# Kernel tuning notes

Measured on AMD Instinct MI355X. Metric: run time of the kernel, lower is better.

## Reference

```python
import jax, jax.numpy as jnp
import numpy as np

D_MODEL = 4096
N_EXPERTS = 64
LN_EPS = 1e-5


def setup_inputs() -> dict:
    key = jax.random.key(0)
    k_x, k_w, k_b = jax.random.split(key, 3)
    x = jax.random.normal(k_x, (4, 4096, D_MODEL), dtype=jnp.float32)
    # LayerNorm affine params (torch defaults: ones / zeros)
    gamma = jnp.ones((D_MODEL,), dtype=jnp.float32)
    beta = jnp.zeros((D_MODEL,), dtype=jnp.float32)
    # Linear(d_model, n): weight (n, d), bias (n) — kaiming-uniform-ish init
    bound = 1.0 / np.sqrt(D_MODEL)
    W = jax.random.uniform(k_w, (N_EXPERTS, D_MODEL), dtype=jnp.float32, minval=-bound, maxval=bound)
    b = jax.random.uniform(k_b, (N_EXPERTS,), dtype=jnp.float32, minval=-bound, maxval=bound)
    return {"x": x, "gamma": gamma, "beta": beta, "W": W, "b": b, "top_k": 2}


def reference(x, gamma, beta, W, b, top_k):
    # LayerNorm over last dim
    mu = jnp.mean(x, axis=-1, keepdims=True)
    var = jnp.mean(jnp.square(x - mu), axis=-1, keepdims=True)
    xn = (x - mu) * jax.lax.rsqrt(var + LN_EPS) * gamma + beta
    # Gate projection: (B,T,d) @ (d,n) -> (B,T,n)
    logits = jnp.einsum('btd,nd->btn', xn, W) + b
    weights = jax.nn.softmax(logits, axis=-1)  # (B,T,n)
    k = min(int(top_k), weights.shape[-1])
    topk_vals, indices = jax.lax.top_k(weights, k)  # (B,T,k)
    # scatter top-k values back to dense (B,T,n), then renormalize
    onehot = jax.nn.one_hot(indices, weights.shape[-1], dtype=weights.dtype)  # (B,T,k,n)
    sparse_w = jnp.einsum('btkn,btk->btn', onehot, topk_vals)
    sparse_w = sparse_w / (jnp.sum(sparse_w, axis=-1, keepdims=True) + 1e-8)
    # load-balance (entropy) loss on dense weights
    mean_w = jnp.mean(weights, axis=(0, 1))  # (n,)
    lb_loss = -jnp.sum(mean_w * jnp.log(mean_w + 1e-8))
    return sparse_w, indices, lb_loss
```

## Files before the change

### kernel.cpp

```cpp
#include <hip/hip_runtime.h>
#include <math.h>

#define D_MODEL 4096
#define N_EXP   64
#define N_ROWS  16384
#define LN_EPS  1e-5f
#define TMB     64
#define NBLK    (N_ROWS / TMB)

typedef __attribute__((ext_vector_type(4))) float f32x4;
typedef __attribute__((ext_vector_type(8))) short s16x8;

struct U4 { unsigned v[4]; };

__device__ __forceinline__ unsigned pkt(float a, float b) {
  unsigned ua = __builtin_bit_cast(unsigned, a);
  unsigned ub = __builtin_bit_cast(unsigned, b);
  return (ua >> 16) | (ub & 0xffff0000u);
}
__device__ __forceinline__ float lo2f(unsigned p) { return __builtin_bit_cast(float, p << 16); }
__device__ __forceinline__ float hi2f(unsigned p) { return __builtin_bit_cast(float, p & 0xffff0000u); }

__device__ __forceinline__ void split8(const float* f, U4& u1, U4& u2, U4& u3) {
#pragma unroll
  for (int i = 0; i < 4; ++i) {
    const float a = f[2 * i], b = f[2 * i + 1];
    const unsigned p1 = pkt(a, b);
    const float ra = a - lo2f(p1), rb = b - hi2f(p1);
    const unsigned p2 = pkt(ra, rb);
    const float sa = ra - lo2f(p2), sb = rb - hi2f(p2);
    u1.v[i] = p1; u2.v[i] = p2; u3.v[i] = pkt(sa, sb);
  }
}


__global__ __launch_bounds__(64) void prep_bpre(
    const float* __restrict__ W, const float* __restrict__ gamma,
    float* __restrict__ Bpre)
{
  const int b = blockIdx.x;
  const int kb32 = b >> 2, j0 = b & 3;
  const int L = threadIdx.x, q = L >> 4, c = L & 15;
  const int n  = j0 * 16 + c;
  const int k0 = kb32 * 32 + q * 8;
  const float4 w0 = *(const float4*)(W + (size_t)n * D_MODEL + k0);
  const float4 w1 = *(const float4*)(W + (size_t)n * D_MODEL + k0 + 4);
  const float4 g0 = *(const float4*)(gamma + k0);
  const float4 g1 = *(const float4*)(gamma + k0 + 4);
  float f[8] = {w0.x * g0.x, w0.y * g0.y, w0.z * g0.z, w0.w * g0.w,
                w1.x * g1.x, w1.y * g1.y, w1.z * g1.z, w1.w * g1.w};
  U4 u1, u2, u3;
  split8(f, u1, u2, u3);
  const size_t base = ((size_t)kb32 * 12 + j0 * 3) * 64 + L;
  *(float4*)(Bpre + (base + 0 * 64) * 4) = __builtin_bit_cast(float4, u1);
  *(float4*)(Bpre + (base + 1 * 64) * 4) = __builtin_bit_cast(float4, u2);
  *(float4*)(Bpre + (base + 2 * 64) * 4) = __builtin_bit_cast(float4, u3);
}

__global__ __launch_bounds__(256) void prep_gc(
    const float* __restrict__ W, const float* __restrict__ gamma,
    const float* __restrict__ beta, const float* __restrict__ bias,
    float* __restrict__ G, float* __restrict__ C)
{
  const int e = blockIdx.x, t = threadIdx.x;
  float sg = 0.f, sb = 0.f;
#pragma unroll
  for (int i = 0; i < 4; ++i) {
    const int d = (i * 256 + t) * 4;
    const float4 wv = *(const float4*)(W + (size_t)e * D_MODEL + d);
    const float4 gv = *(const float4*)(gamma + d);
    const float4 bv = *(const float4*)(beta + d);
    sg += wv.x * gv.x + wv.y * gv.y + wv.z * gv.z + wv.w * gv.w;
    sb += wv.x * bv.x + wv.y * bv.y + wv.z * bv.z + wv.w * bv.w;
  }
#pragma unroll
  for (int o = 32; o > 0; o >>= 1) {
    sg += __shfl_xor(sg, o, 64);
    sb += __shfl_xor(sb, o, 64);
  }
  __shared__ float rg_[4], rb_[4];
  const int wid = t >> 6, ln = t & 63;
  if (ln == 0) { rg_[wid] = sg; rb_[wid] = sb; }
  __syncthreads();
  if (t == 0) {
    G[e] = rg_[0] + rg_[1] + rg_[2] + rg_[3];
    C[e] = rb_[0] + rb_[1] + rb_[2] + rb_[3] + bias[e];
  }
}

__device__ __forceinline__ void loadA(const float* aptr, int kb, float4 A[8]) {
  const float* ap = aptr + (size_t)kb * 128;
#pragma unroll
  for (int s = 0; s < 4; ++s) {
    A[2 * s]     = *(const float4*)(ap + s * 32);
    A[2 * s + 1] = *(const float4*)(ap + s * 32 + 4);
  }
}

__device__ __forceinline__ void gload_lds16(const float* g, const float4* l) {
  __builtin_amdgcn_global_load_lds(
      (const __attribute__((address_space(1))) void*)(g),
      (__attribute__((address_space(3))) void*)(l),
      16, 0, 0);
}

__device__ __forceinline__ void stage_chunk(const float* __restrict__ Bpre,
                                            float4* ldsbuf, int kb, int w, int L)
{
  const float* src = Bpre + (((size_t)(kb * 4 + w) * 12) * 64 + L) * 4;
  float4* dst = ldsbuf + (size_t)(w * 12) * 64;
#pragma unroll
  for (int i = 0; i < 12; ++i)
    gload_lds16(src + (size_t)i * 256, dst + (size_t)i * 64);
}

__device__ __forceinline__ void compute_chunk_lds(
    const float4* __restrict__ buf, int L,
    const float4 Acur[8], f32x4 acc[4], float& Sp, float& Qp)
{
  const int PA[6] = {0, 0, 1, 0, 1, 2};
  const int PB[6] = {0, 1, 0, 2, 1, 0};
#pragma unroll
  for (int s = 0; s < 4; ++s) {
    s16x8 bf[4][3];
#pragma unroll
    for (int j0 = 0; j0 < 4; ++j0)
#pragma unroll
      for (int tt = 0; tt < 3; ++tt)
        bf[j0][tt] = __builtin_bit_cast(s16x8, buf[(size_t)(s * 12 + j0 * 3 + tt) * 64 + L]);
    const float4 a0 = Acur[2 * s], a1 = Acur[2 * s + 1];
    const float f[8] = {a0.x, a0.y, a0.z, a0.w, a1.x, a1.y, a1.z, a1.w};
#pragma unroll
    for (int i = 0; i < 8; ++i) { Sp += f[i]; Qp = fmaf(f[i], f[i], Qp); }
    U4 u1, u2, u3;
    split8(f, u1, u2, u3);
    const s16x8 af[3] = {__builtin_bit_cast(s16x8, u1),
                         __builtin_bit_cast(s16x8, u2),
                         __builtin_bit_cast(s16x8, u3)};
#pragma unroll
    for (int p = 0; p < 6; ++p)
#pragma unroll
      for (int j0 = 0; j0 < 4; ++j0)
        acc[j0] = __builtin_amdgcn_mfma_f32_16x16x32_bf16(af[PA[p]], bf[j0][PB[p]],
                                                          acc[j0], 0, 0, 0);
  }
}

__global__ __launch_bounds__(256, 1) void router_main(
    const float* __restrict__ x, const float* __restrict__ Bpre,
    const float* __restrict__ G, const float* __restrict__ C,
    float* __restrict__ out_sw, float* __restrict__ out_idx,
    float* __restrict__ out_partials, int k)
{
  const int t = threadIdx.x, w = t >> 6, L = t & 63;
  const int q = L >> 4, c = L & 15;
  const int blk = blockIdx.x;
  const int row0 = blk * TMB + w * 16;

  const float* aptr = x + (size_t)(row0 + c) * D_MODEL + q * 8;

  __shared__ float4 Bl[2][48 * 64];

  f32x4 acc[4];
#pragma unroll
  for (int j0 = 0; j0 < 4; ++j0) acc[j0] = (f32x4){0.f, 0.f, 0.f, 0.f};
  float Sp = 0.f, Qp = 0.f;

  float4 A0[8], A1[8];
  loadA(aptr, 0, A0);
  stage_chunk(Bpre, Bl[0], 0, w, L);
  __syncthreads();

  for (int kb = 0; kb < 32; kb += 2) {
    stage_chunk(Bpre, Bl[1], kb + 1, w, L);
    loadA(aptr, kb + 1, A1);
    compute_chunk_lds(Bl[0], L, A0, acc, Sp, Qp);
    __syncthreads();

    if (kb + 2 < 32) stage_chunk(Bpre, Bl[0], kb + 2, w, L);
    loadA(aptr, (kb + 2) & 31, A0);
    compute_chunk_lds(Bl[1], L, A1, acc, Sp, Qp);
    __syncthreads();
  }

#pragma unroll
  for (int o = 16; o <= 32; o <<= 1) {
    Sp += __shfl_xor(Sp, o, 64);
    Qp += __shfl_xor(Qp, o, 64);
  }
  const float mu = Sp * (1.f / D_MODEL);
  const float rs = rsqrtf(Qp * (1.f / D_MODEL) - mu * mu + LN_EPS);

  float Gv[4], Cv[4];
#pragma unroll
  for (int j0 = 0; j0 < 4; ++j0) { Gv[j0] = G[16 * j0 + c]; Cv[j0] = C[16 * j0 + c]; }

  float mw[4] = {0.f, 0.f, 0.f, 0.f};
#pragma unroll
  for (int i = 0; i < 4; ++i) {
    const int rloc = 4 * q + i;
    const int row  = row0 + rloc;
    const float mui = __shfl(mu, rloc, 64);
    const float rsi = __shfl(rs, rloc, 64);
    float l[4];
#pragma unroll
    for (int j0 = 0; j0 < 4; ++j0)
      l[j0] = rsi * (acc[j0][i] - mui * Gv[j0]) + Cv[j0];
    float mx = fmaxf(fmaxf(l[0], l[1]), fmaxf(l[2], l[3]));
#pragma unroll
    for (int o = 1; o < 16; o <<= 1) mx = fmaxf(mx, __shfl_xor(mx, o, 64));
    float p[4], ss = 0.f;
#pragma unroll
    for (int j0 = 0; j0 < 4; ++j0) { p[j0] = __expf(l[j0] - mx); ss += p[j0]; }
#pragma unroll
    for (int o = 1; o < 16; o <<= 1) ss += __shfl_xor(ss, o, 64);
    float wv[4];
#pragma unroll
    for (int j0 = 0; j0 < 4; ++j0) { wv[j0] = p[j0] / ss; mw[j0] += wv[j0]; }

    int ch[4];
    float denom = 0.f;
    for (int kk = 0; kk < k && kk < 4; ++kk) {
      float vb = -1.f; int eb = 1 << 30;
#pragma unroll
      for (int j0 = 0; j0 < 4; ++j0) {
        const int e = 16 * j0 + c;
        bool skip = false;
        for (int z = 0; z < kk; ++z) skip |= (ch[z] == e);
        const float cand = skip ? -1.f : wv[j0];
        if (cand > vb || (cand == vb && e < eb)) { vb = cand; eb = e; }
      }
#pragma unroll
      for (int o = 1; o < 16; o <<= 1) {
        const float ov = __shfl_xor(vb, o, 64);
        const int   oe = __shfl_xor(eb, o, 64);
        if (ov > vb || (ov == vb && oe < eb)) { vb = ov; eb = oe; }
      }
      ch[kk] = eb; denom += vb;
      if (c == 0) out_idx[(size_t)row * k + kk] = (float)eb;
    }
    denom += 1e-8f;
#pragma unroll
    for (int j0 = 0; j0 < 4; ++j0) {
      const int e = 16 * j0 + c;
      bool sel = false;
      for (int z = 0; z < k && z < 4; ++z) sel |= (ch[z] == e);
      out_sw[(size_t)row * N_EXP + e] = sel ? wv[j0] / denom : 0.f;
    }
  }

#pragma unroll
  for (int j0 = 0; j0 < 4; ++j0)
#pragma unroll
    for (int o = 16; o <= 32; o <<= 1) mw[j0] += __shfl_xor(mw[j0], o, 64);
  __shared__ float sm[4][64];
  if (q == 0) {
#pragma unroll
    for (int j0 = 0; j0 < 4; ++j0) sm[w][16 * j0 + c] = mw[j0];
  }
  __syncthreads();
  if (t < 64)
    out_partials[blk * 64 + t] = sm[0][t] + sm[1][t] + sm[2][t] + sm[3][t];
}

__global__ __launch_bounds__(256) void loss_kernel(
    const float* __restrict__ partials, float* __restrict__ out_loss)
{
  const int t = threadIdx.x, e = t & 63, qq = t >> 6;
  float s = 0.f;
#pragma unroll 8
  for (int b = 0; b < 64; ++b) s += partials[(qq * 64 + b) * 64 + e];
  __shared__ float sh[256];
  sh[t] = s;
  __syncthreads();
  if (t < 64) {
    const float m = (sh[t] + sh[64 + t] + sh[128 + t] + sh[192 + t]) * (1.f / N_ROWS);
    float v = -m * logf(m + 1e-8f);
#pragma unroll
    for (int o = 32; o > 0; o >>= 1) v += __shfl_xor(v, o, 64);
    if (t == 0) out_loss[0] = v;
  }
}

extern "C" void kernel_launch(void* const* d_in, const int* in_sizes, int n_in,
                              void* d_out, int out_size, void* d_ws, size_t ws_size,
                              hipStream_t stream)
{
  const float* x     = (const float*)d_in[0];
  const float* gamma = (const float*)d_in[1];
  const float* beta  = (const float*)d_in[2];
  const float* W     = (const float*)d_in[3];
  const float* bias  = (const float*)d_in[4];

  float* ws       = (float*)d_ws;
  float* Bpre     = ws;
  float* G        = ws + 393216;
  float* C        = ws + 393280;
  float* partials = ws + 393344;

  int k = (out_size - N_ROWS * N_EXP - 1) / N_ROWS;
  if (k < 1) k = 1;
  if (k > 4) k = 4;

  float* out      = (float*)d_out;
  float* out_sw   = out;
  float* out_idx  = out + (size_t)N_ROWS * N_EXP;
  float* out_loss = out + (size_t)N_ROWS * N_EXP + (size_t)N_ROWS * k;

  hipLaunchKernelGGL(prep_bpre, dim3(512), dim3(64), 0, stream, W, gamma, Bpre);
  hipLaunchKernelGGL(prep_gc, dim3(N_EXP), dim3(256), 0, stream, W, gamma, beta, bias, G, C);
  hipLaunchKernelGGL(router_main, dim3(NBLK), dim3(256), 0, stream,
                     x, Bpre, G, C, out_sw, out_idx, partials, k);
  hipLaunchKernelGGL(loss_kernel, dim3(1), dim3(256), 0, stream, partials, out_loss);
}
```

Before: 423.2 us.

## Split K dimension across two wave groups per block with LDS reduction

Doubles the block to 512 threads. The two groups of four waves each handle half of the 4096-wide reduction for the same 64 rows, using 64-wide staged chunks. Partial accumulators and LayerNorm sums from the second group are passed through a union of shared memory to the first group, which finishes the softmax/top-k epilogue. This is meant to raise memory-level parallelism and occupancy in the x-streaming GEMM. In exchange it adds an LDS reduction, an extra barrier, and leaves half the waves idle during the epilogue.

```diff
diff --git a/kernel.cpp b/kernel.cpp
--- a/kernel.cpp
+++ b/kernel.cpp
@@ -88,10 +88,10 @@
   }
 }
 
-__device__ __forceinline__ void loadA(const float* aptr, int kb, float4 A[8]) {
-  const float* ap = aptr + (size_t)kb * 128;
-#pragma unroll
-  for (int s = 0; s < 4; ++s) {
+__device__ __forceinline__ void loadA64(const float* aptr, int K0, float4 A[4]) {
+  const float* ap = aptr + K0;
+#pragma unroll
+  for (int s = 0; s < 2; ++s) {
     A[2 * s]     = *(const float4*)(ap + s * 32);
     A[2 * s + 1] = *(const float4*)(ap + s * 32 + 4);
   }
@@ -104,31 +104,31 @@
       16, 0, 0);
 }
 
-__device__ __forceinline__ void stage_chunk(const float* __restrict__ Bpre,
-                                            float4* ldsbuf, int kb, int w, int L)
-{
-  const float* src = Bpre + (((size_t)(kb * 4 + w) * 12) * 64 + L) * 4;
-  float4* dst = ldsbuf + (size_t)(w * 12) * 64;
-#pragma unroll
-  for (int i = 0; i < 12; ++i)
+__device__ __forceinline__ void stage_chunk64(const float* __restrict__ Bpre,
+                                              float4* dstbase, int kb32g, int g, int L)
+{
+  const float* src = Bpre + (((size_t)kb32g * 12 + g * 6) * 64 + L) * 4;
+  float4* dst = dstbase + (size_t)(g * 6) * 64;
+#pragma unroll
+  for (int i = 0; i < 6; ++i)
     gload_lds16(src + (size_t)i * 256, dst + (size_t)i * 64);
 }
 
-__device__ __forceinline__ void compute_chunk_lds(
+__device__ __forceinline__ void compute_chunk64(
     const float4* __restrict__ buf, int L,
-    const float4 Acur[8], f32x4 acc[4], float& Sp, float& Qp)
+    const float4 A[4], f32x4 acc[4], float& Sp, float& Qp)
 {
   const int PA[6] = {0, 0, 1, 0, 1, 2};
   const int PB[6] = {0, 1, 0, 2, 1, 0};
 #pragma unroll
-  for (int s = 0; s < 4; ++s) {
+  for (int s = 0; s < 2; ++s) {
     s16x8 bf[4][3];
 #pragma unroll
     for (int j0 = 0; j0 < 4; ++j0)
 #pragma unroll
       for (int tt = 0; tt < 3; ++tt)
         bf[j0][tt] = __builtin_bit_cast(s16x8, buf[(size_t)(s * 12 + j0 * 3 + tt) * 64 + L]);
-    const float4 a0 = Acur[2 * s], a1 = Acur[2 * s + 1];
+    const float4 a0 = A[2 * s], a1 = A[2 * s + 1];
     const float f[8] = {a0.x, a0.y, a0.z, a0.w, a1.x, a1.y, a1.z, a1.w};
 #pragma unroll
     for (int i = 0; i < 8; ++i) { Sp += f[i]; Qp = fmaf(f[i], f[i], Qp); }
@@ -146,7 +146,7 @@
   }
 }
 
-__global__ __launch_bounds__(256, 1) void router_main(
+__global__ __launch_bounds__(512, 2) void router_main(
     const float* __restrict__ x, const float* __restrict__ Bpre,
     const float* __restrict__ G, const float* __restrict__ C,
     float* __restrict__ out_sw, float* __restrict__ out_idx,
@@ -154,32 +154,40 @@
 {
   const int t = threadIdx.x, w = t >> 6, L = t & 63;
   const int q = L >> 4, c = L & 15;
+  const int g = w & 3;
+  const int ks = w >> 2;
   const int blk = blockIdx.x;
-  const int row0 = blk * TMB + w * 16;
+  const int row0 = blk * TMB + g * 16;
+  const int Kbase = ks * 2048;
+  const int kb32base = ks * 64;
 
   const float* aptr = x + (size_t)(row0 + c) * D_MODEL + q * 8;
 
-  __shared__ float4 Bl[2][48 * 64];
+  union Smem {
+    float4 B[2][2][24 * 64];
+    struct { float red[4][64][19]; float sm[4][64]; } ep;
+  };
+  __shared__ Smem S;
 
   f32x4 acc[4];
 #pragma unroll
   for (int j0 = 0; j0 < 4; ++j0) acc[j0] = (f32x4){0.f, 0.f, 0.f, 0.f};
   float Sp = 0.f, Qp = 0.f;
 
-  float4 A0[8], A1[8];
-  loadA(aptr, 0, A0);
-  stage_chunk(Bpre, Bl[0], 0, w, L);
+  float4 A0[4], A1[4];
+  loadA64(aptr, Kbase, A0);
+  stage_chunk64(Bpre, S.B[ks][0], kb32base, g, L);
   __syncthreads();
 
   for (int kb = 0; kb < 32; kb += 2) {
-    stage_chunk(Bpre, Bl[1], kb + 1, w, L);
-    loadA(aptr, kb + 1, A1);
-    compute_chunk_lds(Bl[0], L, A0, acc, Sp, Qp);
+    stage_chunk64(Bpre, S.B[ks][1], kb32base + (kb + 1) * 2, g, L);
+    loadA64(aptr, Kbase + (kb + 1) * 64, A1);
+    compute_chunk64(S.B[ks][0], L, A0, acc, Sp, Qp);
     __syncthreads();
 
-    if (kb + 2 < 32) stage_chunk(Bpre, Bl[0], kb + 2, w, L);
-    loadA(aptr, (kb + 2) & 31, A0);
-    compute_chunk_lds(Bl[1], L, A1, acc, Sp, Qp);
+    if (kb + 2 < 32) stage_chunk64(Bpre, S.B[ks][0], kb32base + (kb + 2) * 2, g, L);
+    loadA64(aptr, Kbase + ((kb + 2) & 31) * 64, A0);
+    compute_chunk64(S.B[ks][1], L, A1, acc, Sp, Qp);
     __syncthreads();
   }
 
@@ -188,79 +196,98 @@
     Sp += __shfl_xor(Sp, o, 64);
     Qp += __shfl_xor(Qp, o, 64);
   }
-  const float mu = Sp * (1.f / D_MODEL);
-  const float rs = rsqrtf(Qp * (1.f / D_MODEL) - mu * mu + LN_EPS);
-
-  float Gv[4], Cv[4];
-#pragma unroll
-  for (int j0 = 0; j0 < 4; ++j0) { Gv[j0] = G[16 * j0 + c]; Cv[j0] = C[16 * j0 + c]; }
-
-  float mw[4] = {0.f, 0.f, 0.f, 0.f};
-#pragma unroll
-  for (int i = 0; i < 4; ++i) {
-    const int rloc = 4 * q + i;
-    const int row  = row0 + rloc;
-    const float mui = __shfl(mu, rloc, 64);
-    const float rsi = __shfl(rs, rloc, 64);
-    float l[4];
+
+  if (ks == 1) {
+    float* dst = &S.ep.red[g][L][0];
 #pragma unroll
     for (int j0 = 0; j0 < 4; ++j0)
-      l[j0] = rsi * (acc[j0][i] - mui * Gv[j0]) + Cv[j0];
-    float mx = fmaxf(fmaxf(l[0], l[1]), fmaxf(l[2], l[3]));
-#pragma unroll
-    for (int o = 1; o < 16; o <<= 1) mx = fmaxf(mx, __shfl_xor(mx, o, 64));
-    float p[4], ss = 0.f;
-#pragma unroll
-    for (int j0 = 0; j0 < 4; ++j0) { p[j0] = __expf(l[j0] - mx); ss += p[j0]; }
-#pragma unroll
-    for (int o = 1; o < 16; o <<= 1) ss += __shfl_xor(ss, o, 64);
-    float wv[4];
-#pragma unroll
-    for (int j0 = 0; j0 < 4; ++j0) { wv[j0] = p[j0] / ss; mw[j0] += wv[j0]; }
-
-    int ch[4];
-    float denom = 0.f;
-    for (int kk = 0; kk < k && kk < 4; ++kk) {
-      float vb = -1.f; int eb = 1 << 30;
+#pragma unroll
+      for (int i = 0; i < 4; ++i) dst[j0 * 4 + i] = acc[j0][i];
+    dst[16] = Sp; dst[17] = Qp;
+  }
+  __syncthreads();
+
+  if (ks == 0) {
+    const float* sp_ = &S.ep.red[g][L][0];
+#pragma unroll
+    for (int j0 = 0; j0 < 4; ++j0)
+#pragma unroll
+      for (int i = 0; i < 4; ++i) acc[j0][i] += sp_[j0 * 4 + i];
+    Sp += sp_[16]; Qp += sp_[17];
+
+    const float mu = Sp * (1.f / D_MODEL);
+    const float rs = rsqrtf(Qp * (1.f / D_MODEL) - mu * mu + LN_EPS);
+
+    float Gv[4], Cv[4];
+#pragma unroll
+    for (int j0 = 0; j0 < 4; ++j0) { Gv[j0] = G[16 * j0 + c]; Cv[j0] = C[16 * j0 + c]; }
+
+    float mw[4] = {0.f, 0.f, 0.f, 0.f};
+#pragma unroll
+    for (int i = 0; i < 4; ++i) {
+      const int rloc = 4 * q + i;
+      const int row  = row0 + rloc;
+      const float mui = __shfl(mu, rloc, 64);
+      const float rsi = __shfl(rs, rloc, 64);
+      float l[4];
+#pragma unroll
+      for (int j0 = 0; j0 < 4; ++j0)
+        l[j0] = rsi * (acc[j0][i] - mui * Gv[j0]) + Cv[j0];
+      float mx = fmaxf(fmaxf(l[0], l[1]), fmaxf(l[2], l[3]));
+#pragma unroll
+      for (int o = 1; o < 16; o <<= 1) mx = fmaxf(mx, __shfl_xor(mx, o, 64));
+      float p[4], ss = 0.f;
+#pragma unroll
+      for (int j0 = 0; j0 < 4; ++j0) { p[j0] = __expf(l[j0] - mx); ss += p[j0]; }
+#pragma unroll
+      for (int o = 1; o < 16; o <<= 1) ss += __shfl_xor(ss, o, 64);
+      float wv[4];
+#pragma unroll
+      for (int j0 = 0; j0 < 4; ++j0) { wv[j0] = p[j0] / ss; mw[j0] += wv[j0]; }
+
+      int ch[4];
+      float denom = 0.f;
+      for (int kk = 0; kk < k && kk < 4; ++kk) {
+        float vb = -1.f; int eb = 1 << 30;
+#pragma unroll
+        for (int j0 = 0; j0 < 4; ++j0) {
+          const int e = 16 * j0 + c;
+          bool skip = false;
+          for (int z = 0; z < kk; ++z) skip |= (ch[z] == e);
+          const float cand = skip ? -1.f : wv[j0];
+          if (cand > vb || (cand == vb && e < eb)) { vb = cand; eb = e; }
+        }
+#pragma unroll
+        for (int o = 1; o < 16; o <<= 1) {
+          const float ov = __shfl_xor(vb, o, 64);
+          const int   oe = __shfl_xor(eb, o, 64);
+          if (ov > vb || (ov == vb && oe < eb)) { vb = ov; eb = oe; }
+        }
+        ch[kk] = eb; denom += vb;
+        if (c == 0) out_idx[(size_t)row * k + kk] = (float)eb;
+      }
+      denom += 1e-8f;
 #pragma unroll
       for (int j0 = 0; j0 < 4; ++j0) {
         const int e = 16 * j0 + c;
-        bool skip = false;
-        for (int z = 0; z < kk; ++z) skip |= (ch[z] == e);
-        const float cand = skip ? -1.f : wv[j0];
-        if (cand > vb || (cand == vb && e < eb)) { vb = cand; eb = e; }
+        bool sel = false;
+        for (int z = 0; z < k && z < 4; ++z) sel |= (ch[z] == e);
+        out_sw[(size_t)row * N_EXP + e] = sel ? wv[j0] / denom : 0.f;
       }
-#pragma unroll
-      for (int o = 1; o < 16; o <<= 1) {
-        const float ov = __shfl_xor(vb, o, 64);
-        const int   oe = __shfl_xor(eb, o, 64);
-        if (ov > vb || (ov == vb && oe < eb)) { vb = ov; eb = oe; }
-      }
-      ch[kk] = eb; denom += vb;
-      if (c == 0) out_idx[(size_t)row * k + kk] = (float)eb;
     }
-    denom += 1e-8f;
-#pragma unroll
-    for (int j0 = 0; j0 < 4; ++j0) {
-      const int e = 16 * j0 + c;
-      bool sel = false;
-      for (int z = 0; z < k && z < 4; ++z) sel |= (ch[z] == e);
-      out_sw[(size_t)row * N_EXP + e] = sel ? wv[j0] / denom : 0.f;
+
+#pragma unroll
+    for (int j0 = 0; j0 < 4; ++j0)
+#pragma unroll
+      for (int o = 16; o <= 32; o <<= 1) mw[j0] += __shfl_xor(mw[j0], o, 64);
+    if (q == 0) {
+#pragma unroll
+      for (int j0 = 0; j0 < 4; ++j0) S.ep.sm[g][16 * j0 + c] = mw[j0];
     }
   }
-
-#pragma unroll
-  for (int j0 = 0; j0 < 4; ++j0)
-#pragma unroll
-    for (int o = 16; o <= 32; o <<= 1) mw[j0] += __shfl_xor(mw[j0], o, 64);
-  __shared__ float sm[4][64];
-  if (q == 0) {
-#pragma unroll
-    for (int j0 = 0; j0 < 4; ++j0) sm[w][16 * j0 + c] = mw[j0];
-  }
   __syncthreads();
   if (t < 64)
-    out_partials[blk * 64 + t] = sm[0][t] + sm[1][t] + sm[2][t] + sm[3][t];
+    out_partials[blk * 64 + t] = S.ep.sm[0][t] + S.ep.sm[1][t] + S.ep.sm[2][t] + S.ep.sm[3][t];
 }
 
 __global__ __launch_bounds__(256) void loss_kernel(
@@ -309,7 +336,7 @@
 
   hipLaunchKernelGGL(prep_bpre, dim3(512), dim3(64), 0, stream, W, gamma, Bpre);
   hipLaunchKernelGGL(prep_gc, dim3(N_EXP), dim3(256), 0, stream, W, gamma, beta, bias, G, C);
-  hipLaunchKernelGGL(router_main, dim3(NBLK), dim3(256), 0, stream,
+  hipLaunchKernelGGL(router_main, dim3(NBLK), dim3(512), 0, stream,
                      x, Bpre, G, C, out_sw, out_idx, partials, k);
   hipLaunchKernelGGL(loss_kernel, dim3(1), dim3(256), 0, stream, partials, out_loss);
 }
```

Result: no change. 421.4 us (-0.4%).
